# Performance work log

Measured on AMD Instinct MI355X. Metric: run time of the kernel, lower is better.

## Reference

```python
import math
import jax, jax.numpy as jnp
import numpy as np

N_HEAD = 16

def setup_inputs() -> dict:
    key = jax.random.key(0)
    ks = jax.random.split(key, 3)
    B, T, C = 2, 2048, 1024
    x = jax.random.normal(ks[0], (B, T, C), dtype=jnp.float32)
    W_attn = jax.random.normal(ks[1], (3 * C, C), dtype=jnp.float32) * (1.0 / math.sqrt(C))
    b_attn = jnp.zeros((3 * C,), dtype=jnp.float32)
    W_proj = jax.random.normal(ks[2], (C, C), dtype=jnp.float32) * (1.0 / math.sqrt(C))
    b_proj = jnp.zeros((C,), dtype=jnp.float32)
    return {"x": x, "W_attn": W_attn, "b_attn": b_attn, "W_proj": W_proj, "b_proj": b_proj}

def reference(x, W_attn, b_attn, W_proj, b_proj):
    B, T, C = x.shape
    H = N_HEAD
    Dh = C // H
    qkv = x @ W_attn.T + b_attn                      # [B,T,3C]
    q, k, v = jnp.split(qkv, 3, axis=-1)
    q = q.reshape(B, T, H, Dh).transpose(0, 2, 1, 3)  # [B,H,T,Dh]
    k = k.reshape(B, T, H, Dh).transpose(0, 2, 1, 3)
    v = v.reshape(B, T, H, Dh).transpose(0, 2, 1, 3)
    att = jnp.einsum('bhqd,bhkd->bhqk', q, k) * (1.0 / math.sqrt(Dh))
    # ALiBi-style RPE: bias[h, r, c] = -(r - c) * 2^(-8/H * (h+1)) for c <= r, 0 above diag
    rows = jnp.arange(T)[:, None]
    cols = jnp.arange(T)[None, :]
    dist = jnp.minimum((cols - rows).astype(jnp.float32), 0.0)  # [T,T]
    slopes = 2.0 ** (-8.0 / H * (jnp.arange(H, dtype=jnp.float32) + 1.0))  # [H]
    att = att + slopes[None, :, None, None] * dist[None, None]
    causal = cols <= rows                              # [T,T]
    att = jnp.where(causal[None, None], att, -jnp.inf)
    att = jax.nn.softmax(att, axis=-1)                 # dropout p=0.0 -> identity
    y = jnp.einsum('bhqk,bhkd->bhqd', att, v)          # [B,H,T,Dh]
    y = y.transpose(0, 2, 1, 3).reshape(B, T, C)
    y = y @ W_proj.T + b_proj
    return y
```

## Files before the change

kernel.cpp:

```cpp
#include <hip/hip_runtime.h>

typedef __bf16 bf16x8 __attribute__((ext_vector_type(8)));
typedef __bf16 bf16x4 __attribute__((ext_vector_type(4)));
typedef float  f32x4  __attribute__((ext_vector_type(4)));
typedef float  f32x16 __attribute__((ext_vector_type(16)));

#define TSEQ 2048
#define CDIM 1024
#define NHEAD 16
#define DH 64
#define SCALE2 0.1803368801111137f

__device__ __forceinline__ void gl_lds16(const void* g, void* l) {
  __builtin_amdgcn_global_load_lds(
      (const __attribute__((address_space(1))) unsigned int*)g,
      (__attribute__((address_space(3))) unsigned int*)l, 16, 0, 0);
}

__device__ __forceinline__ float fexp2(float x) { return __builtin_amdgcn_exp2f(x); }

__device__ __forceinline__ unsigned cvtpk(float a, float b) {
  unsigned r;
  asm("v_cvt_pk_bf16_f32 %0, %1, %2" : "=v"(r) : "v"(a), "v"(b));
  return r;
}
__device__ __forceinline__ void permswap(unsigned& x, unsigned& y) {
  asm("v_permlane32_swap_b32 %0, %1" : "+v"(x), "+v"(y));
}

__device__ __forceinline__ float tsum16(const f32x16& s) {
  float a0 = s[0] + s[1], a1 = s[2] + s[3], a2 = s[4] + s[5], a3 = s[6] + s[7];
  float a4 = s[8] + s[9], a5 = s[10] + s[11], a6 = s[12] + s[13], a7 = s[14] + s[15];
  float b0 = a0 + a1, b1 = a2 + a3, b2 = a4 + a5, b3 = a6 + a7;
  return (b0 + b1) + (b2 + b3);
}

__global__ __launch_bounds__(256) void cvt_bf16_all(
    const float* __restrict__ x, const float* __restrict__ wa,
    const float* __restrict__ wp, __bf16* __restrict__ xb,
    __bf16* __restrict__ wab, __bf16* __restrict__ wpb) {
  int i = blockIdx.x * 256 + threadIdx.x;
  const float* in;
  __bf16* out;
  int off;
  if (i < 524288)      { in = x;  out = xb;  off = i; }
  else if (i < 917504) { in = wa; out = wab; off = i - 524288; }
  else                 { in = wp; out = wpb; off = i - 917504; }
  const float4* p = (const float4*)(in + (size_t)off * 8);
  float4 a = p[0], b = p[1];
  bf16x8 r;
  r[0] = (__bf16)a.x; r[1] = (__bf16)a.y; r[2] = (__bf16)a.z; r[3] = (__bf16)a.w;
  r[4] = (__bf16)b.x; r[5] = (__bf16)b.y; r[6] = (__bf16)b.z; r[7] = (__bf16)b.w;
  *(bf16x8*)(out + (size_t)off * 8) = r;
}

__global__ __launch_bounds__(256) void gemm_qkv(
    const __bf16* __restrict__ A, const __bf16* __restrict__ Bw,
    const float* __restrict__ bias,
    __bf16* __restrict__ q_pack, __bf16* __restrict__ k_pack,
    __bf16* __restrict__ v_pack, int K) {
  __shared__ alignas(16) __bf16 lda[128 * 64];
  __shared__ alignas(16) __bf16 ldb[128 * 64];
  const int tid = threadIdx.x;
  const int lane = tid & 63, wid = tid >> 6;
  const int wm = wid >> 1, wn = wid & 1;
  const int row0 = blockIdx.y * 128, col0 = blockIdx.x * 128;
  f32x4 acc[4][4] = {};

  const int srow = lane >> 3;
  const int scb = ((lane & 7) ^ (lane >> 3)) * 16;

  for (int k0 = 0; k0 < K; k0 += 64) {
#pragma unroll
    for (int j = 0; j < 4; ++j) {
      int blk = j * 4 + wid;
      int r = blk * 8 + srow;
      char* la = (char*)lda + blk * 1024;
      char* lb = (char*)ldb + blk * 1024;
      gl_lds16((const char*)(A + (size_t)(row0 + r) * K + k0) + scb, la);
      gl_lds16((const char*)(Bw + (size_t)(col0 + r) * K + k0) + scb, lb);
    }
    __syncthreads();
#pragma unroll
    for (int kk = 0; kk < 2; ++kk) {
      const int sl = (((kk << 2) | (lane >> 4)) ^ (lane & 7)) * 16;
      bf16x8 af[4], bfr[4];
#pragma unroll
      for (int m = 0; m < 4; ++m)
        af[m] = *(const bf16x8*)((const char*)lda +
                                 (wm * 64 + m * 16 + (lane & 15)) * 128 + sl);
#pragma unroll
      for (int n = 0; n < 4; ++n)
        bfr[n] = *(const bf16x8*)((const char*)ldb +
                                  (wn * 64 + n * 16 + (lane & 15)) * 128 + sl);
#pragma unroll
      for (int m = 0; m < 4; ++m)
#pragma unroll
        for (int n = 0; n < 4; ++n)
          acc[m][n] = __builtin_amdgcn_mfma_f32_16x16x32_bf16(af[m], bfr[n], acc[m][n], 0, 0, 0);
    }
    __syncthreads();
  }
#pragma unroll
  for (int m = 0; m < 4; ++m) {
#pragma unroll
    for (int n = 0; n < 4; ++n) {
#pragma unroll
      for (int i = 0; i < 4; ++i) {
        int r = row0 + wm * 64 + m * 16 + (lane >> 4) * 4 + i;
        int c = col0 + wn * 64 + n * 16 + (lane & 15);
        float v = acc[m][n][i] + bias[c];
        int bb = r >> 11, t = r & 2047;
        int sec = c >> 10, cc = c & 1023;
        int hh = cc >> 6, d = cc & 63;
        size_t bh = (size_t)bb * NHEAD + hh;
        if (sec == 2) {
          int j = t >> 5, kh = (t >> 4) & 1, half = d >> 5;
          int l2 = (d & 31) + ((t >> 3) & 1) * 32, e = t & 7;
          v_pack[(bh * 256 + (size_t)(j * 4 + kh * 2 + half)) * 512 + l2 * 8 + e] = (__bf16)v;
        } else {
          int ch = t >> 5, mm = d >> 4;
          int l2 = (t & 31) + ((d >> 3) & 1) * 32, e = d & 7;
          size_t idx = ((bh * 64 + ch) * 4 + (size_t)mm) * 512 + l2 * 8 + e;
          if (sec == 0) q_pack[idx] = (__bf16)(v * SCALE2);
          else          k_pack[idx] = (__bf16)v;
        }
      }
    }
  }
}

__global__ __launch_bounds__(256) void gemm_proj(
    const __bf16* __restrict__ A, const __bf16* __restrict__ Bw,
    const float* __restrict__ bias, float* __restrict__ outf) {
  const int K = CDIM, N = CDIM;
  __shared__ alignas(16) __bf16 lda[64 * 64];
  __shared__ alignas(16) __bf16 ldb[128 * 64];
  const int tid = threadIdx.x;
  const int lane = tid & 63, wid = tid >> 6;
  const int row0 = blockIdx.y * 64, col0 = blockIdx.x * 128;
  f32x4 acc[4][2] = {};

  const int srow = lane >> 3;
  const int scb = ((lane & 7) ^ (lane >> 3)) * 16;

  for (int k0 = 0; k0 < K; k0 += 64) {
#pragma unroll
    for (int j = 0; j < 2; ++j) {
      int blk = j * 4 + wid;
      gl_lds16((const char*)(A + (size_t)(row0 + blk * 8 + srow) * K + k0) + scb,
               (char*)lda + blk * 1024);
    }
#pragma unroll
    for (int j = 0; j < 4; ++j) {
      int blk = j * 4 + wid;
      gl_lds16((const char*)(Bw + (size_t)(col0 + blk * 8 + srow) * K + k0) + scb,
               (char*)ldb + blk * 1024);
    }
    __syncthreads();
#pragma unroll
    for (int kk = 0; kk < 2; ++kk) {
      const int sl = (((kk << 2) | (lane >> 4)) ^ (lane & 7)) * 16;
      bf16x8 af[4], bfr[2];
#pragma unroll
      for (int m = 0; m < 4; ++m)
        af[m] = *(const bf16x8*)((const char*)lda + (m * 16 + (lane & 15)) * 128 + sl);
#pragma unroll
      for (int n = 0; n < 2; ++n)
        bfr[n] = *(const bf16x8*)((const char*)ldb +
                                  (wid * 32 + n * 16 + (lane & 15)) * 128 + sl);
#pragma unroll
      for (int m = 0; m < 4; ++m)
#pragma unroll
        for (int n = 0; n < 2; ++n)
          acc[m][n] = __builtin_amdgcn_mfma_f32_16x16x32_bf16(af[m], bfr[n], acc[m][n], 0, 0, 0);
    }
    __syncthreads();
  }
#pragma unroll
  for (int m = 0; m < 4; ++m) {
#pragma unroll
    for (int n = 0; n < 2; ++n) {
#pragma unroll
      for (int i = 0; i < 4; ++i) {
        int r = row0 + m * 16 + (lane >> 4) * 4 + i;
        int c = col0 + wid * 32 + n * 16 + (lane & 15);
        outf[(size_t)r * N + c] = acc[m][n][i] + bias[c];
      }
    }
  }
}

__device__ __forceinline__ void softmax_pv(
    f32x16& s, bool domask, int lq, int hi,
    float& l_r, f32x16& o0, f32x16& o1,
    const bf16x8* va0, const bf16x8* va1) {
#pragma unroll
  for (int r = 0; r < 16; ++r) s[r] = fexp2(s[r]);
  if (domask) {
#pragma unroll
    for (int r = 0; r < 16; ++r) {
      int kof = (r & 3) + 8 * (r >> 2) + 4 * hi;
      if (kof > lq) s[r] = 0.f;
    }
  }
  l_r += tsum16(s);
  bf16x8 pb[2];
#pragma unroll
  for (int kh = 0; kh < 2; ++kh) {
    const int bq = kh * 8;
    unsigned w0 = cvtpk(s[bq + 0], s[bq + 1]);
    unsigned w1 = cvtpk(s[bq + 2], s[bq + 3]);
    unsigned w2 = cvtpk(s[bq + 4], s[bq + 5]);
    unsigned w3 = cvtpk(s[bq + 6], s[bq + 7]);
    permswap(w0, w2);
    permswap(w1, w3);
    union { unsigned u[4]; bf16x8 v; } pbu;
    pbu.u[0] = w0; pbu.u[1] = w1; pbu.u[2] = w2; pbu.u[3] = w3;
    pb[kh] = pbu.v;
  }
  o0 = __builtin_amdgcn_mfma_f32_32x32x16_bf16(va0[0], pb[0], o0, 0, 0, 0);
  o0 = __builtin_amdgcn_mfma_f32_32x32x16_bf16(va0[1], pb[1], o0, 0, 0, 0);
  o1 = __builtin_amdgcn_mfma_f32_32x32x16_bf16(va1[0], pb[0], o1, 0, 0, 0);
  o1 = __builtin_amdgcn_mfma_f32_32x32x16_bf16(va1[1], pb[1], o1, 0, 0, 0);
}

__global__ __launch_bounds__(64) void attn_fwd(
    const __bf16* __restrict__ q_pack, const __bf16* __restrict__ k_pack,
    const __bf16* __restrict__ v_pack, __bf16* __restrict__ y_buf) {
  const int lane = threadIdx.x;
  const int lq = lane & 31;
  const int hi = lane >> 5;
  const int bh = blockIdx.x;
  const int wv = blockIdx.y;
  const int b = bh >> 4, h = bh & 15;
  const int cH = 63 - wv, cL = wv;
  const float slope2 = exp2f(-0.5f * (float)(h + 1)) * 1.44269504f;
  const __bf16* qpk = q_pack + (size_t)bh * 64 * 2048;
  const __bf16* kpk = k_pack + (size_t)bh * 64 * 2048;
  const __bf16* vpk = v_pack + (size_t)bh * 64 * 2048;
  const int lo = lane * 8;

  bf16x8 qfH[4], qfL[4];
#pragma unroll
  for (int m = 0; m < 4; ++m) {
    qfH[m] = *(const bf16x8*)&qpk[(size_t)(cH * 4 + m) * 512 + lo];
    qfL[m] = *(const bf16x8*)&qpk[(size_t)(cL * 4 + m) * 512 + lo];
  }
  float pk_[16];
#pragma unroll
  for (int r = 0; r < 16; ++r)
    pk_[r] = slope2 * (float)((r & 3) + 8 * (r >> 2) + 4 * hi);

  f32x16 oH0 = {}, oH1 = {}, oL0 = {}, oL1 = {};
  float lH = 0.f, lL = 0.f;

  bf16x8 kf[4];
#pragma unroll
  for (int m = 0; m < 4; ++m)
    kf[m] = *(const bf16x8*)&kpk[(size_t)m * 512 + lo];

  for (int j = 0; j <= cH; ++j) {
    const int kt = j * 32;
    bf16x8 va0[2], va1[2];
#pragma unroll
    for (int kh = 0; kh < 2; ++kh) {
      va0[kh] = *(const bf16x8*)&vpk[(size_t)(j * 4 + kh * 2 + 0) * 512 + lo];
      va1[kh] = *(const bf16x8*)&vpk[(size_t)(j * 4 + kh * 2 + 1) * 512 + lo];
    }
    bf16x8 kn[4];
    const bool pre = (j < cH);
    if (pre) {
#pragma unroll
      for (int m = 0; m < 4; ++m)
        kn[m] = *(const bf16x8*)&kpk[(size_t)((j + 1) * 4 + m) * 512 + lo];
    }
    const float bH = slope2 * (float)(kt - cH * 32);
    f32x16 sH;
#pragma unroll
    for (int r = 0; r < 16; ++r) sH[r] = pk_[r] + bH;
#pragma unroll
    for (int m = 0; m < 4; ++m)
      sH = __builtin_amdgcn_mfma_f32_32x32x16_bf16(kf[m], qfH[m], sH, 0, 0, 0);
    const bool lact = (j <= cL);
    f32x16 sL;
    if (lact) {
      const float bL = slope2 * (float)(kt - cL * 32);
#pragma unroll
      for (int r = 0; r < 16; ++r) sL[r] = pk_[r] + bL;
#pragma unroll
      for (int m = 0; m < 4; ++m)
        sL = __builtin_amdgcn_mfma_f32_32x32x16_bf16(kf[m], qfL[m], sL, 0, 0, 0);
    }
    softmax_pv(sH, j == cH, lq, hi, lH, oH0, oH1, va0, va1);
    if (lact)
      softmax_pv(sL, j == cL, lq, hi, lL, oL0, oL1, va0, va1);
    if (pre) {
#pragma unroll
      for (int m = 0; m < 4; ++m) kf[m] = kn[m];
    }
  }
  lH += __shfl_xor(lH, 32, 64);
  lL += __shfl_xor(lL, 32, 64);

#pragma unroll
  for (int g2 = 0; g2 < 2; ++g2) {
    const int c = g2 ? cL : cH;
    const f32x16& a0 = g2 ? oL0 : oH0;
    const f32x16& a1 = g2 ? oL1 : oH1;
    const float inv = 1.0f / (g2 ? lL : lH);
    __bf16* yb = y_buf + ((size_t)b * TSEQ + c * 32 + lq) * CDIM + h * DH;
#pragma unroll
    for (int g = 0; g < 4; ++g) {
      bf16x4 v0, v1;
#pragma unroll
      for (int e = 0; e < 4; ++e) {
        v0[e] = (__bf16)(a0[4 * g + e] * inv);
        v1[e] = (__bf16)(a1[4 * g + e] * inv);
      }
      *(bf16x4*)&yb[8 * g + 4 * hi] = v0;
      *(bf16x4*)&yb[32 + 8 * g + 4 * hi] = v1;
    }
  }
}

extern "C" void kernel_launch(void* const* d_in, const int* in_sizes, int n_in,
                              void* d_out, int out_size, void* d_ws, size_t ws_size,
                              hipStream_t stream) {
  const float* x      = (const float*)d_in[0];
  const float* W_attn = (const float*)d_in[1];
  const float* b_attn = (const float*)d_in[2];
  const float* W_proj = (const float*)d_in[3];
  const float* b_proj = (const float*)d_in[4];
  float* out = (float*)d_out;
  char* ws = (char*)d_ws;
  const size_t MB = (size_t)1 << 20;
  __bf16* xb  = (__bf16*)(ws + 0 * MB);
  __bf16* wab = (__bf16*)(ws + 8 * MB);
  __bf16* wpb = (__bf16*)(ws + 14 * MB);
  __bf16* qpk = (__bf16*)(ws + 16 * MB);
  __bf16* kpk = (__bf16*)(ws + 24 * MB);
  __bf16* vpk = (__bf16*)(ws + 32 * MB);
  __bf16* yb  = (__bf16*)(ws + 40 * MB);

  cvt_bf16_all<<<4096, 256, 0, stream>>>(x, W_attn, W_proj, xb, wab, wpb);

  gemm_qkv<<<dim3(24, 32), 256, 0, stream>>>(xb, wab, b_attn, qpk, kpk, vpk, 1024);
  attn_fwd<<<dim3(32, 32), 64, 0, stream>>>(qpk, kpk, vpk, yb);
  gemm_proj<<<dim3(8, 64), 256, 0, stream>>>(yb, wpb, b_proj, out);
}
```

Before: 114.5 us.

## Compute softmax row sums with ones-MFMA and swizzle GEMM block order

Replaces the per-lane 16-element VALU tree sum and cross-half shuffle used for the softmax denominator with two extra MFMAs that multiply a ones matrix by the bf16 probability tile. The denominator is now accumulated from the same bf16-rounded P values used in the PV product. Separately, both GEMM kernels remap block indices so that consecutive workgroups are spread across tiles, aiming for better L2/MALL reuse across XCDs. The MFMA route adds matrix work and 16 accumulator registers per tile set to take VALU work off the attention inner loop.

New measurement: 115.0 us. No clear change (+0.5%).

```diff
diff --git a/kernel.cpp b/kernel.cpp
--- a/kernel.cpp
+++ b/kernel.cpp
@@ -26,13 +26,6 @@
 }
 __device__ __forceinline__ void permswap(unsigned& x, unsigned& y) {
   asm("v_permlane32_swap_b32 %0, %1" : "+v"(x), "+v"(y));
-}
-
-__device__ __forceinline__ float tsum16(const f32x16& s) {
-  float a0 = s[0] + s[1], a1 = s[2] + s[3], a2 = s[4] + s[5], a3 = s[6] + s[7];
-  float a4 = s[8] + s[9], a5 = s[10] + s[11], a6 = s[12] + s[13], a7 = s[14] + s[15];
-  float b0 = a0 + a1, b1 = a2 + a3, b2 = a4 + a5, b3 = a6 + a7;
-  return (b0 + b1) + (b2 + b3);
 }
 
 __global__ __launch_bounds__(256) void cvt_bf16_all(
@@ -64,7 +57,9 @@
   const int tid = threadIdx.x;
   const int lane = tid & 63, wid = tid >> 6;
   const int wm = wid >> 1, wn = wid & 1;
-  const int row0 = blockIdx.y * 128, col0 = blockIdx.x * 128;
+  const int hw = (int)(blockIdx.x + 24 * blockIdx.y);
+  const int logi = (hw & 7) * 96 + (hw >> 3);
+  const int row0 = (logi / 24) * 128, col0 = (logi % 24) * 128;
   f32x4 acc[4][4] = {};
 
   const int srow = lane >> 3;
@@ -138,7 +133,9 @@
   __shared__ alignas(16) __bf16 ldb[128 * 64];
   const int tid = threadIdx.x;
   const int lane = tid & 63, wid = tid >> 6;
-  const int row0 = blockIdx.y * 64, col0 = blockIdx.x * 128;
+  const int hw = (int)(blockIdx.x + 8 * blockIdx.y);
+  const int logi = (hw & 7) * 64 + (hw >> 3);
+  const int row0 = (logi / 8) * 64, col0 = (logi % 8) * 128;
   f32x4 acc[4][2] = {};
 
   const int srow = lane >> 3;
@@ -192,8 +189,8 @@
 }
 
 __device__ __forceinline__ void softmax_pv(
-    f32x16& s, bool domask, int lq, int hi,
-    float& l_r, f32x16& o0, f32x16& o1,
+    f32x16& s, bool domask, int lq, int hi, bf16x8 ones,
+    f32x16& lones, f32x16& o0, f32x16& o1,
     const bf16x8* va0, const bf16x8* va1) {
 #pragma unroll
   for (int r = 0; r < 16; ++r) s[r] = fexp2(s[r]);
@@ -204,7 +201,6 @@
       if (kof > lq) s[r] = 0.f;
     }
   }
-  l_r += tsum16(s);
   bf16x8 pb[2];
 #pragma unroll
   for (int kh = 0; kh < 2; ++kh) {
@@ -223,6 +219,8 @@
   o0 = __builtin_amdgcn_mfma_f32_32x32x16_bf16(va0[1], pb[1], o0, 0, 0, 0);
   o1 = __builtin_amdgcn_mfma_f32_32x32x16_bf16(va1[0], pb[0], o1, 0, 0, 0);
   o1 = __builtin_amdgcn_mfma_f32_32x32x16_bf16(va1[1], pb[1], o1, 0, 0, 0);
+  lones = __builtin_amdgcn_mfma_f32_32x32x16_bf16(ones, pb[0], lones, 0, 0, 0);
+  lones = __builtin_amdgcn_mfma_f32_32x32x16_bf16(ones, pb[1], lones, 0, 0, 0);
 }
 
 __global__ __launch_bounds__(64) void attn_fwd(
@@ -241,6 +239,10 @@
   const __bf16* vpk = v_pack + (size_t)bh * 64 * 2048;
   const int lo = lane * 8;
 
+  bf16x8 ones;
+#pragma unroll
+  for (int e = 0; e < 8; ++e) ones[e] = (__bf16)1.0f;
+
   bf16x8 qfH[4], qfL[4];
 #pragma unroll
   for (int m = 0; m < 4; ++m) {
@@ -253,7 +255,7 @@
     pk_[r] = slope2 * (float)((r & 3) + 8 * (r >> 2) + 4 * hi);
 
   f32x16 oH0 = {}, oH1 = {}, oL0 = {}, oL1 = {};
-  float lH = 0.f, lL = 0.f;
+  f32x16 lnH = {}, lnL = {};
 
   bf16x8 kf[4];
 #pragma unroll
@@ -292,23 +294,21 @@
       for (int m = 0; m < 4; ++m)
         sL = __builtin_amdgcn_mfma_f32_32x32x16_bf16(kf[m], qfL[m], sL, 0, 0, 0);
     }
-    softmax_pv(sH, j == cH, lq, hi, lH, oH0, oH1, va0, va1);
+    softmax_pv(sH, j == cH, lq, hi, ones, lnH, oH0, oH1, va0, va1);
     if (lact)
-      softmax_pv(sL, j == cL, lq, hi, lL, oL0, oL1, va0, va1);
+      softmax_pv(sL, j == cL, lq, hi, ones, lnL, oL0, oL1, va0, va1);
     if (pre) {
 #pragma unroll
       for (int m = 0; m < 4; ++m) kf[m] = kn[m];
     }
   }
-  lH += __shfl_xor(lH, 32, 64);
-  lL += __shfl_xor(lL, 32, 64);
 
 #pragma unroll
   for (int g2 = 0; g2 < 2; ++g2) {
     const int c = g2 ? cL : cH;
     const f32x16& a0 = g2 ? oL0 : oH0;
     const f32x16& a1 = g2 ? oL1 : oH1;
-    const float inv = 1.0f / (g2 ? lL : lH);
+    const float inv = 1.0f / (g2 ? lnL[0] : lnH[0]);
     __bf16* yb = y_buf + ((size_t)b * TSEQ + c * 32 + lq) * CDIM + h * DH;
 #pragma unroll
     for (int g = 0; g < 4; ++g) {
```
